# Kernel optimization log

Hardware: AMD Instinct MI355X
Metric: run time of the kernel (lower is better)

The kernel has to match this reference:

```python
import jax, jax.numpy as jnp
import numpy as np
import math

B, L, DIM = 2, 2048, 1024
HEADS = 16
DH = DIM // HEADS  # 64
M_IALSH = 2
U_IALSH = 0.75
NEG = -1e4  # additive mask value for non-matching hash buckets


def setup_inputs() -> dict:
    key = jax.random.key(0)
    k0, k1, k2, k3 = jax.random.split(key, 4)
    return {
        "hidden_states": jax.random.normal(k0, (B, L, DIM), jnp.float32),
        "qk_w": jax.random.normal(k1, (DIM, DIM), jnp.float32) * 0.02,
        "qk_b": jnp.zeros((DIM,), jnp.float32),
        "v_w": jax.random.normal(k2, (DIM, DIM), jnp.float32) * 0.02,
        "v_b": jnp.zeros((DIM,), jnp.float32),
        "hash_a": jax.random.normal(k3, (DH + M_IALSH,), jnp.float32),
    }


def _ialsh_mask(qkh, hash_a):
    # qkh: (b, h, l, dh). IALSH (Improved Asymmetric LSH for MIPS):
    # keys scaled so max norm per (b,h) is U; P(x)=[x, 1/2-||x||^2, 1/2-||x||^4]
    # queries unit-normalized;        Q(x)=[x/||x||, 0, 0]
    norms = jnp.linalg.norm(qkh, axis=-1, keepdims=True)          # (b,h,l,1)
    max_norm = jnp.max(norms, axis=2, keepdims=True)              # (b,h,1,1)
    xk = qkh * (U_IALSH / jnp.maximum(max_norm, 1e-12))
    nk2 = jnp.sum(xk * xk, axis=-1, keepdims=True)                # ||x||^2
    P = jnp.concatenate([xk, 0.5 - nk2, 0.5 - nk2 * nk2], axis=-1)
    q_unit = qkh / jnp.maximum(norms, 1e-12)
    zeros = jnp.zeros_like(nk2)
    Q = jnp.concatenate([q_unit, zeros, zeros], axis=-1)
    hq = (Q @ hash_a) >= 0.0                                      # (b,h,l) sign hash
    hk = (P @ hash_a) >= 0.0
    same = hq[..., :, None] == hk[..., None, :]                   # (b,h,l,l)
    return jnp.where(same, 0.0, NEG).astype(qkh.dtype)


def reference(hidden_states, qk_w, qk_b, v_w, v_b, hash_a):
    b, l, d = hidden_states.shape
    qk = hidden_states @ qk_w.T + qk_b                            # shared Q/K projection
    v = hidden_states @ v_w.T + v_b

    def split(x):  # (b,l,d) -> (b,h,l,dh)
        return x.reshape(b, l, HEADS, DH).transpose(0, 2, 1, 3)

    qkh, vh = split(qk), split(v)
    scores = jnp.einsum('bhqd,bhkd->bhqk', qkh, qkh) / math.sqrt(DH)
    scores = scores + _ialsh_mask(qkh, hash_a)
    probs = jax.nn.softmax(scores, axis=-1)  # dropout = identity (eval mode)
    ctx = jnp.einsum('bhqk,bhkd->bhqd', probs, vh)
    return ctx.transpose(0, 2, 1, 3).reshape(b, l, d)
```

## Files before the change

kernel.cpp:

```cpp
#include <hip/hip_runtime.h>

typedef unsigned short u16;
typedef unsigned char  u8;
typedef unsigned int   u32;

typedef short bf16x8 __attribute__((ext_vector_type(8)));
typedef float f32x4  __attribute__((ext_vector_type(4)));

#define DEV __device__ __forceinline__

#if __has_builtin(__builtin_amdgcn_exp2f)
#define EXP2(x) __builtin_amdgcn_exp2f(x)
#else
#define EXP2(x) exp2f(x)
#endif

DEV u16 f2bf(float x) {
  u32 u = __builtin_bit_cast(u32, x);
  u32 r = (u + 0x7fffu + ((u >> 16) & 1u)) >> 16;
  return (u16)r;
}
DEV float bf2f(u16 h) {
  u32 u = ((u32)h) << 16;
  return __builtin_bit_cast(float, u);
}
DEV f32x4 mfma16(bf16x8 a, bf16x8 b, f32x4 c) {
  return __builtin_amdgcn_mfma_f32_16x16x32_bf16(a, b, c, 0, 0, 0);
}

__global__ __launch_bounds__(256) void split_kernel(
    const float* __restrict__ x, u16* __restrict__ hi, u16* __restrict__ lo, int n) {
  int i = blockIdx.x * 256 + threadIdx.x;
  if (i >= n) return;
  float v = x[i];
  u16 h = f2bf(v);
  hi[i] = h;
  lo[i] = f2bf(v - bf2f(h));
}

__global__ __launch_bounds__(256) void ca_kernel(
    const float* __restrict__ W, const float* __restrict__ ha, double* __restrict__ ca) {
  int idx = blockIdx.x * 256 + threadIdx.x;
  int h = idx >> 10, k = idx & 1023;
  double s = 0.0;
#pragma unroll 8
  for (int j = 0; j < 64; ++j)
    s += (double)W[(size_t)(h * 64 + j) * 1024 + k] * (double)ha[j];
  ca[idx] = s;
}

__global__ __launch_bounds__(256) void d_kernel(
    const float* __restrict__ hid, const double* __restrict__ ca, float* __restrict__ dq) {
  const int row  = blockIdx.x * 4 + (threadIdx.x >> 6);
  const int lane = threadIdx.x & 63;
  const int b = row >> 11, l = row & 2047;
  double acc[16];
#pragma unroll
  for (int h = 0; h < 16; ++h) acc[h] = 0.0;
  const float* hp = hid + (size_t)row * 1024;
  for (int k = lane; k < 1024; k += 64) {
    const double hv = (double)hp[k];
#pragma unroll
    for (int h = 0; h < 16; ++h) acc[h] += hv * ca[h * 1024 + k];
  }
#pragma unroll
  for (int h = 0; h < 16; ++h) {
    double v = acc[h];
#pragma unroll
    for (int off = 32; off; off >>= 1) v += __shfl_xor(v, off, 64);
    if (lane == 0) dq[(size_t)(b * 16 + h) * 2048 + l] = (float)v;
  }
}

__global__ __launch_bounds__(256) void gemm_fused(
    const u16* __restrict__ hHi, const u16* __restrict__ hLo,
    const u16* __restrict__ wqHi, const u16* __restrict__ wqLo,
    const u16* __restrict__ wvHi,
    const float* __restrict__ qk_b, const float* __restrict__ v_b,
    u16* __restrict__ qkB, u16* __restrict__ vB, float* __restrict__ n2A) {
  constexpr int K = 1024, N = 1024;
  __shared__ u16 Ah[128 * 32];
  __shared__ u16 Bh[128 * 32];
  __shared__ u16 Al[128 * 32];
  __shared__ u16 Bl[128 * 32];

  const int zsel = blockIdx.z;
  const u16* __restrict__ Ahi = hHi;
  const u16* __restrict__ Bhi = zsel ? wvHi : wqHi;
  const float* __restrict__ bias = zsel ? v_b : qk_b;
  u16* __restrict__ Cb = zsel ? vB : qkB;
  const int terms = zsel ? 1 : 3;

  const int tid = threadIdx.x;
  const int wave = tid >> 6, lane = tid & 63;
  const int quad = lane >> 4, lm = lane & 15;
  const int wr = wave >> 1, wc = wave & 1;
  const int m0 = blockIdx.x * 128, n0 = blockIdx.y * 128;

  f32x4 acc[4][4];
#pragma unroll
  for (int i = 0; i < 4; ++i)
#pragma unroll
    for (int j = 0; j < 4; ++j) acc[i][j] = {0.f, 0.f, 0.f, 0.f};

  for (int k0 = 0; k0 < K; k0 += 32) {
    __syncthreads();
#pragma unroll
    for (int it = 0; it < 2; ++it) {
      const int rb = wave * 2 + it;
      const int row = rb * 16 + (lane >> 2);
      const int ch = lane & 3;
      const size_t goffA = (size_t)(m0 + row) * K + k0 + ch * 8;
      const size_t goffB = (size_t)(n0 + row) * K + k0 + ch * 8;
      __builtin_amdgcn_global_load_lds(
          (const __attribute__((address_space(1))) void*)(Ahi + goffA),
          (__attribute__((address_space(3))) void*)(Ah + rb * 512), 16, 0, 0);
      __builtin_amdgcn_global_load_lds(
          (const __attribute__((address_space(1))) void*)(Bhi + goffB),
          (__attribute__((address_space(3))) void*)(Bh + rb * 512), 16, 0, 0);
      if (terms > 1) {
        __builtin_amdgcn_global_load_lds(
            (const __attribute__((address_space(1))) void*)(hLo + goffA),
            (__attribute__((address_space(3))) void*)(Al + rb * 512), 16, 0, 0);
        __builtin_amdgcn_global_load_lds(
            (const __attribute__((address_space(1))) void*)(wqLo + goffB),
            (__attribute__((address_space(3))) void*)(Bl + rb * 512), 16, 0, 0);
      }
    }
    __syncthreads();

    bf16x8 a_h[4], b_h[4], a_l[4], b_l[4];
#pragma unroll
    for (int i = 0; i < 4; ++i)
      a_h[i] = *(const bf16x8*)(Ah + (wr * 64 + i * 16 + lm) * 32 + quad * 8);
#pragma unroll
    for (int j = 0; j < 4; ++j)
      b_h[j] = *(const bf16x8*)(Bh + (wc * 64 + j * 16 + lm) * 32 + quad * 8);
    if (terms > 1) {
#pragma unroll
      for (int i = 0; i < 4; ++i)
        a_l[i] = *(const bf16x8*)(Al + (wr * 64 + i * 16 + lm) * 32 + quad * 8);
#pragma unroll
      for (int j = 0; j < 4; ++j)
        b_l[j] = *(const bf16x8*)(Bl + (wc * 64 + j * 16 + lm) * 32 + quad * 8);
    }
    if (terms > 1) {
#pragma unroll
      for (int i = 0; i < 4; ++i)
#pragma unroll
        for (int j = 0; j < 4; ++j) {
          acc[i][j] = mfma16(a_h[i], b_h[j], acc[i][j]);
          acc[i][j] = mfma16(a_h[i], b_l[j], acc[i][j]);
          acc[i][j] = mfma16(a_l[i], b_h[j], acc[i][j]);
        }
    } else {
#pragma unroll
      for (int i = 0; i < 4; ++i)
#pragma unroll
        for (int j = 0; j < 4; ++j)
          acc[i][j] = mfma16(a_h[i], b_h[j], acc[i][j]);
    }
  }

  const int hidx = blockIdx.y * 2 + wc;
#pragma unroll
  for (int i = 0; i < 4; ++i) {
    float nn[4] = {0.f, 0.f, 0.f, 0.f};
#pragma unroll
    for (int j = 0; j < 4; ++j) {
      const int col = n0 + wc * 64 + j * 16 + lm;
      const float bv = bias[col];
#pragma unroll
      for (int r = 0; r < 4; ++r) {
        const int row = m0 + wr * 64 + i * 16 + quad * 4 + r;
        const float val = acc[i][j][r] + bv;
        Cb[(size_t)row * N + col] = f2bf(val);
        nn[r] += val * val;
      }
    }
    if (zsel == 0) {
#pragma unroll
      for (int r = 0; r < 4; ++r)
#pragma unroll
        for (int off = 1; off < 16; off <<= 1) nn[r] += __shfl_xor(nn[r], off, 64);
      if (lm == 0) {
        const int row = m0 + wr * 64 + i * 16 + quad * 4;
        const int b = row >> 11, l = row & 2047;
        *(float4*)&n2A[(size_t)(b * 16 + hidx) * 2048 + l] =
            make_float4(nn[0], nn[1], nn[2], nn[3]);
      }
    }
  }
}

__global__ __launch_bounds__(256) void vtrans_kernel(
    const u16* __restrict__ vB, u16* __restrict__ vT) {
  constexpr int TS = 72;
  __shared__ u16 Ts[64 * TS];
  const int kt = blockIdx.x, bh = blockIdx.y;
  const int b = bh >> 4, h = bh & 15;
  const int tid = threadIdx.x;
  const int row0 = tid >> 3, ch = tid & 7;
  const u16* src = vB + (size_t)b * 2048 * 1024 + h * 64;
#pragma unroll
  for (int it = 0; it < 2; ++it) {
    const int kr = row0 + it * 32;
    uint4 v = *(const uint4*)(src + (size_t)(kt * 64 + kr) * 1024 + ch * 8);
    *(uint4*)((char*)Ts + kr * (TS * 2) + ch * 16) = v;
  }
  __syncthreads();
  u16* dst = vT + (size_t)bh * 64 * 2048 + kt * 64;
#pragma unroll
  for (int it = 0; it < 2; ++it) {
    const int d = row0 + it * 32;
    union { uint4 v; u16 s[8]; } u;
#pragma unroll
    for (int j = 0; j < 8; ++j) u.s[j] = Ts[(ch * 8 + j) * TS + d];
    *(uint4*)(dst + (size_t)d * 2048 + ch * 8) = u.v;
  }
}

__global__ __launch_bounds__(256) void bits_kernel(
    const float* __restrict__ n2A, const float* __restrict__ dq,
    const float* __restrict__ ha, u8* __restrict__ hqA, u8* __restrict__ hkA) {
  const int bh = blockIdx.x;
  const int tid = threadIdx.x;
  const int wave = tid >> 6, lane = tid & 63;
  __shared__ float red[4];
  const float* n2p = n2A + (size_t)bh * 2048;
  float4 v0 = ((const float4*)n2p)[tid];
  float4 v1 = ((const float4*)n2p)[tid + 256];
  float lmax = fmaxf(fmaxf(fmaxf(v0.x, v0.y), fmaxf(v0.z, v0.w)),
                     fmaxf(fmaxf(v1.x, v1.y), fmaxf(v1.z, v1.w)));
#pragma unroll
  for (int off = 1; off < 64; off <<= 1) lmax = fmaxf(lmax, __shfl_xor(lmax, off, 64));
  if (lane == 0) red[wave] = lmax;
  __syncthreads();
  const float maxn2 = fmaxf(fmaxf(red[0], red[1]), fmaxf(red[2], red[3]));
  const float s = 0.75f / fmaxf(sqrtf(maxn2), 1e-12f);
  const float a64 = ha[64], a65 = ha[65];
#pragma unroll
  for (int it = 0; it < 8; ++it) {
    const int l = it * 256 + tid;
    const float dv = dq[(size_t)bh * 2048 + l];
    const float n2 = n2p[l];
    const float nk2 = s * s * n2;
    const float hkdot = s * dv + (0.5f - nk2) * a64 + (0.5f - nk2 * nk2) * a65;
    hqA[(size_t)bh * 2048 + l] = (dv >= 0.f) ? 1 : 0;
    hkA[(size_t)bh * 2048 + l] = (hkdot >= 0.f) ? 1 : 0;
  }
}

__global__ __launch_bounds__(256, 3) void attn_kernel(
    const u16* __restrict__ qkb, const u16* __restrict__ vT,
    const u8* __restrict__ hqA, const u8* __restrict__ hkA, float* __restrict__ out) {
  __shared__ u16 Ks[2][4096];
  __shared__ u16 Vs[2][4096];
  __shared__ u16 Ps[4][2048];

  const int qt = blockIdx.x;
  const int bh = blockIdx.y;
  const int b = bh >> 4, h = bh & 15;
  const int tid = threadIdx.x, wave = tid >> 6, lane = tid & 63;
  const int quad = lane >> 4, lm = lane & 15;
  const int lx = lm & 7;
  const int r8 = lane >> 3, ch = lane & 7;
  const int q0 = qt * 128;

  const u16* qbase = qkb + (size_t)b * 2048 * 1024 + h * 64;
  const u16* vtb = vT + (size_t)bh * 64 * 2048;
  const u8* hkp = hkA + (size_t)bh * 2048;

  bf16x8 aQ[2][2];
#pragma unroll
  for (int s = 0; s < 2; ++s)
#pragma unroll
    for (int c = 0; c < 2; ++c)
      aQ[s][c] = *(const bf16x8*)(qbase +
          (size_t)(q0 + wave * 32 + s * 16 + lm) * 1024 + c * 32 + quad * 8);
  u8 hqb[2][4];
  {
    const u8* hqp = hqA + (size_t)bh * 2048 + q0 + wave * 32;
#pragma unroll
    for (int s = 0; s < 2; ++s)
#pragma unroll
      for (int r = 0; r < 4; ++r) hqb[s][r] = hqp[s * 16 + quad * 4 + r];
  }

  const int srow = wave * 16;
  auto stage = [&](int kt, int buf) {
#pragma unroll
    for (int i = 0; i < 2; ++i) {
      const int row = srow + i * 8 + r8;
      const int sw = (ch ^ (row & 7)) * 8;
      __builtin_amdgcn_global_load_lds(
          (const __attribute__((address_space(1))) void*)(
              qbase + (size_t)(kt * 64 + row) * 1024 + sw),
          (__attribute__((address_space(3))) void*)(&Ks[buf][(srow + i * 8) * 64]),
          16, 0, 0);
      __builtin_amdgcn_global_load_lds(
          (const __attribute__((address_space(1))) void*)(
              vtb + (size_t)row * 2048 + kt * 64 + sw),
          (__attribute__((address_space(3))) void*)(&Vs[buf][(srow + i * 8) * 64]),
          16, 0, 0);
    }
  };

  stage(0, 0);

  f32x4 acc_o[2][4], accL[2];
#pragma unroll
  for (int s = 0; s < 2; ++s) {
    accL[s] = {0.f, 0.f, 0.f, 0.f};
#pragma unroll
    for (int j = 0; j < 4; ++j) acc_o[s][j] = {0.f, 0.f, 0.f, 0.f};
  }
  const bf16x8 ones = {0x3F80, 0x3F80, 0x3F80, 0x3F80, 0x3F80, 0x3F80, 0x3F80, 0x3F80};
  const float SCL = 0.18033688f;
  const float M0 = -4.3280854f;
  const float M1 = -1.4430768e4f;

  __syncthreads();

  for (int kt = 0; kt < 32; ++kt) {
    const int cur = kt & 1;
    if (kt < 31) stage(kt + 1, cur ^ 1);

    u8 hkv[4];
#pragma unroll
    for (int nb = 0; nb < 4; ++nb) hkv[nb] = hkp[kt * 64 + nb * 16 + lm];

    f32x4 cs[2][4];
#pragma unroll
    for (int s = 0; s < 2; ++s)
#pragma unroll
      for (int nb = 0; nb < 4; ++nb) cs[s][nb] = {0.f, 0.f, 0.f, 0.f};
#pragma unroll
    for (int c = 0; c < 2; ++c)
#pragma unroll
      for (int nb = 0; nb < 4; ++nb) {
        bf16x8 bK = *(const bf16x8*)&Ks[cur][(nb * 16 + lm) * 64 + (((c * 4 + quad) ^ lx) * 8)];
        cs[0][nb] = mfma16(aQ[0][c], bK, cs[0][nb]);
        cs[1][nb] = mfma16(aQ[1][c], bK, cs[1][nb]);
      }

#pragma unroll
    for (int s = 0; s < 2; ++s)
#pragma unroll
      for (int nb = 0; nb < 4; ++nb)
#pragma unroll
        for (int r = 0; r < 4; ++r) {
          const float msel = (hqb[s][r] == hkv[nb]) ? M0 : M1;
          const float p = EXP2(__builtin_fmaf(cs[s][nb][r], SCL, msel));
          const int prow = s * 16 + quad * 4 + r;
          const int pc = (nb * 2 + (lm >> 3)) ^ (prow & 7);
          union { float f; u16 hw[2]; } u;
          u.f = p;
          Ps[wave][prow * 64 + pc * 8 + lx] = u.hw[1];
        }

    bf16x8 aP[2][2];
#pragma unroll
    for (int s = 0; s < 2; ++s)
#pragma unroll
      for (int c = 0; c < 2; ++c) {
        aP[s][c] = *(const bf16x8*)&Ps[wave][(s * 16 + lm) * 64 + (((c * 4 + quad) ^ lx) * 8)];
        accL[s] = mfma16(aP[s][c], ones, accL[s]);
      }
#pragma unroll
    for (int c = 0; c < 2; ++c)
#pragma unroll
      for (int j = 0; j < 4; ++j) {
        bf16x8 bV = *(const bf16x8*)&Vs[cur][(j * 16 + lm) * 64 + (((c * 4 + quad) ^ lx) * 8)];
        acc_o[0][j] = mfma16(aP[0][c], bV, acc_o[0][j]);
        acc_o[1][j] = mfma16(aP[1][c], bV, acc_o[1][j]);
      }

    __syncthreads();
  }

#pragma unroll
  for (int s = 0; s < 2; ++s)
#pragma unroll
    for (int r = 0; r < 4; ++r) {
      const float inv = 1.0f / accL[s][r];
      float* op = out + (size_t)(b * 2048 + q0 + wave * 32 + s * 16 + quad * 4 + r) * 1024 + h * 64;
#pragma unroll
      for (int j = 0; j < 4; ++j) op[j * 16 + lm] = acc_o[s][j][r] * inv;
    }
}

extern "C" void kernel_launch(void* const* d_in, const int* in_sizes, int n_in,
                              void* d_out, int out_size, void* d_ws, size_t ws_size,
                              hipStream_t stream) {
  const float* hidden = (const float*)d_in[0];
  const float* qk_w   = (const float*)d_in[1];
  const float* qk_b   = (const float*)d_in[2];
  const float* v_w    = (const float*)d_in[3];
  const float* v_b    = (const float*)d_in[4];
  const float* hash_a = (const float*)d_in[5];
  float* out = (float*)d_out;

  char* base = (char*)d_ws;
  size_t off = 0;
  auto take = [&](size_t bytes) -> char* {
    char* r = base + off;
    off += (bytes + 255) & ~(size_t)255;
    return r;
  };
  const size_t NH = 4194304;
  const size_t NW = 1048576;
  u16* hHi  = (u16*)take(NH * 2);
  u16* hLo  = (u16*)take(NH * 2);
  u16* wqHi = (u16*)take(NW * 2);
  u16* wqLo = (u16*)take(NW * 2);
  u16* wvHi = (u16*)take(NW * 2);
  u16* wvLo = (u16*)take(NW * 2);
  u16* qkB  = (u16*)take(NH * 2);
  u16* vB   = (u16*)take(NH * 2);
  u16* vT   = (u16*)take(NH * 2);
  double* ca = (double*)take(16 * 1024 * 8);
  float* dq  = (float*)take(65536 * 4);
  float* n2A = (float*)take(65536 * 4);
  u8* hqA = (u8*)take(65536);
  u8* hkA = (u8*)take(65536);

  hipLaunchKernelGGL(split_kernel, dim3(NH / 256), dim3(256), 0, stream, hidden, hHi, hLo, (int)NH);
  hipLaunchKernelGGL(split_kernel, dim3(NW / 256), dim3(256), 0, stream, qk_w, wqHi, wqLo, (int)NW);
  hipLaunchKernelGGL(split_kernel, dim3(NW / 256), dim3(256), 0, stream, v_w, wvHi, wvLo, (int)NW);
  hipLaunchKernelGGL(ca_kernel, dim3(64), dim3(256), 0, stream, qk_w, hash_a, ca);
  hipLaunchKernelGGL(d_kernel, dim3(1024), dim3(256), 0, stream, hidden, ca, dq);
  hipLaunchKernelGGL(gemm_fused, dim3(32, 8, 2), dim3(256), 0, stream,
                     hHi, hLo, wqHi, wqLo, wvHi, qk_b, v_b, qkB, vB, n2A);
  hipLaunchKernelGGL(vtrans_kernel, dim3(32, 32), dim3(256), 0, stream, vB, vT);
  hipLaunchKernelGGL(bits_kernel, dim3(32), dim3(256), 0, stream, n2A, dq, hash_a, hqA, hkA);
  hipLaunchKernelGGL(attn_kernel, dim3(16, 32), dim3(256), 0, stream, qkB, vT, hqA, hkA, out);
}
```

Baseline: 257.0 us.

## Compute V transposed directly in GEMM and halve attention query tile

```diff
diff --git a/kernel.cpp b/kernel.cpp
--- a/kernel.cpp
+++ b/kernel.cpp
@@ -77,25 +77,26 @@
     const u16* __restrict__ wqHi, const u16* __restrict__ wqLo,
     const u16* __restrict__ wvHi,
     const float* __restrict__ qk_b, const float* __restrict__ v_b,
-    u16* __restrict__ qkB, u16* __restrict__ vB, float* __restrict__ n2A) {
-  constexpr int K = 1024, N = 1024;
+    u16* __restrict__ qkB, u16* __restrict__ vT, float* __restrict__ n2A) {
+  constexpr int K = 1024;
   __shared__ u16 Ah[128 * 32];
   __shared__ u16 Bh[128 * 32];
   __shared__ u16 Al[128 * 32];
   __shared__ u16 Bl[128 * 32];
 
   const int zsel = blockIdx.z;
-  const u16* __restrict__ Ahi = hHi;
-  const u16* __restrict__ Bhi = zsel ? wvHi : wqHi;
-  const float* __restrict__ bias = zsel ? v_b : qk_b;
-  u16* __restrict__ Cb = zsel ? vB : qkB;
+  const int m0 = (zsel ? blockIdx.y : blockIdx.x) * 128;
+  const int n0 = (zsel ? blockIdx.x : blockIdx.y) * 128;
+  const int CN = zsel ? 4096 : 1024;
+  const u16* __restrict__ Ahi = zsel ? wvHi : hHi;
+  const u16* __restrict__ Bhi = zsel ? hHi : wqHi;
+  u16* __restrict__ Cb = zsel ? vT : qkB;
   const int terms = zsel ? 1 : 3;
 
   const int tid = threadIdx.x;
   const int wave = tid >> 6, lane = tid & 63;
   const int quad = lane >> 4, lm = lane & 15;
   const int wr = wave >> 1, wc = wave & 1;
-  const int m0 = blockIdx.x * 128, n0 = blockIdx.y * 128;
 
   f32x4 acc[4][4];
 #pragma unroll
@@ -143,8 +144,6 @@
 #pragma unroll
       for (int j = 0; j < 4; ++j)
         b_l[j] = *(const bf16x8*)(Bl + (wc * 64 + j * 16 + lm) * 32 + quad * 8);
-    }
-    if (terms > 1) {
 #pragma unroll
       for (int i = 0; i < 4; ++i)
 #pragma unroll
@@ -162,23 +161,23 @@
     }
   }
 
-  const int hidx = blockIdx.y * 2 + wc;
-#pragma unroll
-  for (int i = 0; i < 4; ++i) {
-    float nn[4] = {0.f, 0.f, 0.f, 0.f};
-#pragma unroll
-    for (int j = 0; j < 4; ++j) {
-      const int col = n0 + wc * 64 + j * 16 + lm;
-      const float bv = bias[col];
-#pragma unroll
-      for (int r = 0; r < 4; ++r) {
-        const int row = m0 + wr * 64 + i * 16 + quad * 4 + r;
-        const float val = acc[i][j][r] + bv;
-        Cb[(size_t)row * N + col] = f2bf(val);
-        nn[r] += val * val;
-      }
-    }
-    if (zsel == 0) {
+  if (zsel == 0) {
+    const int hidx = blockIdx.y * 2 + wc;
+#pragma unroll
+    for (int i = 0; i < 4; ++i) {
+      float nn[4] = {0.f, 0.f, 0.f, 0.f};
+#pragma unroll
+      for (int j = 0; j < 4; ++j) {
+        const int col = n0 + wc * 64 + j * 16 + lm;
+        const float bv = qk_b[col];
+#pragma unroll
+        for (int r = 0; r < 4; ++r) {
+          const int row = m0 + wr * 64 + i * 16 + quad * 4 + r;
+          const float val = acc[i][j][r] + bv;
+          Cb[(size_t)row * CN + col] = f2bf(val);
+          nn[r] += val * val;
+        }
+      }
 #pragma unroll
       for (int r = 0; r < 4; ++r)
 #pragma unroll
@@ -190,33 +189,19 @@
             make_float4(nn[0], nn[1], nn[2], nn[3]);
       }
     }
-  }
-}
-
-__global__ __launch_bounds__(256) void vtrans_kernel(
-    const u16* __restrict__ vB, u16* __restrict__ vT) {
-  constexpr int TS = 72;
-  __shared__ u16 Ts[64 * TS];
-  const int kt = blockIdx.x, bh = blockIdx.y;
-  const int b = bh >> 4, h = bh & 15;
-  const int tid = threadIdx.x;
-  const int row0 = tid >> 3, ch = tid & 7;
-  const u16* src = vB + (size_t)b * 2048 * 1024 + h * 64;
-#pragma unroll
-  for (int it = 0; it < 2; ++it) {
-    const int kr = row0 + it * 32;
-    uint4 v = *(const uint4*)(src + (size_t)(kt * 64 + kr) * 1024 + ch * 8);
-    *(uint4*)((char*)Ts + kr * (TS * 2) + ch * 16) = v;
-  }
-  __syncthreads();
-  u16* dst = vT + (size_t)bh * 64 * 2048 + kt * 64;
-#pragma unroll
-  for (int it = 0; it < 2; ++it) {
-    const int d = row0 + it * 32;
-    union { uint4 v; u16 s[8]; } u;
-#pragma unroll
-    for (int j = 0; j < 8; ++j) u.s[j] = Ts[(ch * 8 + j) * TS + d];
-    *(uint4*)(dst + (size_t)d * 2048 + ch * 8) = u.v;
+  } else {
+#pragma unroll
+    for (int i = 0; i < 4; ++i)
+#pragma unroll
+      for (int r = 0; r < 4; ++r) {
+        const int row = m0 + wr * 64 + i * 16 + quad * 4 + r;
+        const float bv = v_b[row];
+#pragma unroll
+        for (int j = 0; j < 4; ++j) {
+          const int col = n0 + wc * 64 + j * 16 + lm;
+          Cb[(size_t)row * CN + col] = f2bf(acc[i][j][r] + bv);
+        }
+      }
   }
 }
 
@@ -251,12 +236,12 @@
   }
 }
 
-__global__ __launch_bounds__(256, 3) void attn_kernel(
+__global__ __launch_bounds__(256, 4) void attn_kernel(
     const u16* __restrict__ qkb, const u16* __restrict__ vT,
     const u8* __restrict__ hqA, const u8* __restrict__ hkA, float* __restrict__ out) {
   __shared__ u16 Ks[2][4096];
   __shared__ u16 Vs[2][4096];
-  __shared__ u16 Ps[4][2048];
+  __shared__ u16 Ps[4][1024];
 
   const int qt = blockIdx.x;
   const int bh = blockIdx.y;
@@ -265,26 +250,22 @@
   const int quad = lane >> 4, lm = lane & 15;
   const int lx = lm & 7;
   const int r8 = lane >> 3, ch = lane & 7;
-  const int q0 = qt * 128;
+  const int q0 = qt * 64;
 
   const u16* qbase = qkb + (size_t)b * 2048 * 1024 + h * 64;
-  const u16* vtb = vT + (size_t)bh * 64 * 2048;
+  const u16* vtb = vT + (size_t)h * 64 * 4096 + b * 2048;
   const u8* hkp = hkA + (size_t)bh * 2048;
 
-  bf16x8 aQ[2][2];
-#pragma unroll
-  for (int s = 0; s < 2; ++s)
-#pragma unroll
-    for (int c = 0; c < 2; ++c)
-      aQ[s][c] = *(const bf16x8*)(qbase +
-          (size_t)(q0 + wave * 32 + s * 16 + lm) * 1024 + c * 32 + quad * 8);
-  u8 hqb[2][4];
+  bf16x8 aQ[2];
+#pragma unroll
+  for (int c = 0; c < 2; ++c)
+    aQ[c] = *(const bf16x8*)(qbase +
+        (size_t)(q0 + wave * 16 + lm) * 1024 + c * 32 + quad * 8);
+  u8 hqb[4];
   {
-    const u8* hqp = hqA + (size_t)bh * 2048 + q0 + wave * 32;
-#pragma unroll
-    for (int s = 0; s < 2; ++s)
-#pragma unroll
-      for (int r = 0; r < 4; ++r) hqb[s][r] = hqp[s * 16 + quad * 4 + r];
+    const u8* hqp = hqA + (size_t)bh * 2048 + q0 + wave * 16;
+#pragma unroll
+    for (int r = 0; r < 4; ++r) hqb[r] = hqp[quad * 4 + r];
   }
 
   const int srow = wave * 16;
@@ -300,7 +281,7 @@
           16, 0, 0);
       __builtin_amdgcn_global_load_lds(
           (const __attribute__((address_space(1))) void*)(
-              vtb + (size_t)row * 2048 + kt * 64 + sw),
+              vtb + (size_t)row * 4096 + kt * 64 + sw),
           (__attribute__((address_space(3))) void*)(&Vs[buf][(srow + i * 8) * 64]),
           16, 0, 0);
     }
@@ -308,13 +289,10 @@
 
   stage(0, 0);
 
-  f32x4 acc_o[2][4], accL[2];
-#pragma unroll
-  for (int s = 0; s < 2; ++s) {
-    accL[s] = {0.f, 0.f, 0.f, 0.f};
-#pragma unroll
-    for (int j = 0; j < 4; ++j) acc_o[s][j] = {0.f, 0.f, 0.f, 0.f};
-  }
+  f32x4 acc_o[4], accL;
+  accL = {0.f, 0.f, 0.f, 0.f};
+#pragma unroll
+  for (int j = 0; j < 4; ++j) acc_o[j] = {0.f, 0.f, 0.f, 0.f};
   const bf16x8 ones = {0x3F80, 0x3F80, 0x3F80, 0x3F80, 0x3F80, 0x3F80, 0x3F80, 0x3F80};
   const float SCL = 0.18033688f;
   const float M0 = -4.3280854f;
@@ -330,64 +308,54 @@
 #pragma unroll
     for (int nb = 0; nb < 4; ++nb) hkv[nb] = hkp[kt * 64 + nb * 16 + lm];
 
-    f32x4 cs[2][4];
-#pragma unroll
-    for (int s = 0; s < 2; ++s)
-#pragma unroll
-      for (int nb = 0; nb < 4; ++nb) cs[s][nb] = {0.f, 0.f, 0.f, 0.f};
+    f32x4 cs[4];
+#pragma unroll
+    for (int nb = 0; nb < 4; ++nb) cs[nb] = {0.f, 0.f, 0.f, 0.f};
 #pragma unroll
     for (int c = 0; c < 2; ++c)
 #pragma unroll
       for (int nb = 0; nb < 4; ++nb) {
         bf16x8 bK = *(const bf16x8*)&Ks[cur][(nb * 16 + lm) * 64 + (((c * 4 + quad) ^ lx) * 8)];
-        cs[0][nb] = mfma16(aQ[0][c], bK, cs[0][nb]);
-        cs[1][nb] = mfma16(aQ[1][c], bK, cs[1][nb]);
-      }
-
-#pragma unroll
-    for (int s = 0; s < 2; ++s)
-#pragma unroll
-      for (int nb = 0; nb < 4; ++nb)
-#pragma unroll
-        for (int r = 0; r < 4; ++r) {
-          const float msel = (hqb[s][r] == hkv[nb]) ? M0 : M1;
-          const float p = EXP2(__builtin_fmaf(cs[s][nb][r], SCL, msel));
-          const int prow = s * 16 + quad * 4 + r;
-          const int pc = (nb * 2 + (lm >> 3)) ^ (prow & 7);
-          union { float f; u16 hw[2]; } u;
-          u.f = p;
-          Ps[wave][prow * 64 + pc * 8 + lx] = u.hw[1];
-        }
-
-    bf16x8 aP[2][2];
-#pragma unroll
-    for (int s = 0; s < 2; ++s)
-#pragma unroll
-      for (int c = 0; c < 2; ++c) {
-        aP[s][c] = *(const bf16x8*)&Ps[wave][(s * 16 + lm) * 64 + (((c * 4 + quad) ^ lx) * 8)];
-        accL[s] = mfma16(aP[s][c], ones, accL[s]);
-      }
+        cs[nb] = mfma16(aQ[c], bK, cs[nb]);
+      }
+
+#pragma unroll
+    for (int nb = 0; nb < 4; ++nb)
+#pragma unroll
+      for (int r = 0; r < 4; ++r) {
+        const float msel = (hqb[r] == hkv[nb]) ? M0 : M1;
+        const float p = EXP2(__builtin_fmaf(cs[nb][r], SCL, msel));
+        const int prow = quad * 4 + r;
+        const int pc = (nb * 2 + (lm >> 3)) ^ (prow & 7);
+        union { float f; u16 hw[2]; } u;
+        u.f = p;
+        Ps[wave][prow * 64 + pc * 8 + lx] = u.hw[1];
+      }
+
+    bf16x8 aP[2];
+#pragma unroll
+    for (int c = 0; c < 2; ++c) {
+      aP[c] = *(const bf16x8*)&Ps[wave][lm * 64 + (((c * 4 + quad) ^ lx) * 8)];
+      accL = mfma16(aP[c], ones, accL);
+    }
 #pragma unroll
     for (int c = 0; c < 2; ++c)
 #pragma unroll
       for (int j = 0; j < 4; ++j) {
         bf16x8 bV = *(const bf16x8*)&Vs[cur][(j * 16 + lm) * 64 + (((c * 4 + quad) ^ lx) * 8)];
-        acc_o[0][j] = mfma16(aP[0][c], bV, acc_o[0][j]);
-        acc_o[1][j] = mfma16(aP[1][c], bV, acc_o[1][j]);
+        acc_o[j] = mfma16(aP[c], bV, acc_o[j]);
       }
 
     __syncthreads();
   }
 
 #pragma unroll
-  for (int s = 0; s < 2; ++s)
-#pragma unroll
-    for (int r = 0; r < 4; ++r) {
-      const float inv = 1.0f / accL[s][r];
-      float* op = out + (size_t)(b * 2048 + q0 + wave * 32 + s * 16 + quad * 4 + r) * 1024 + h * 64;
-#pragma unroll
-      for (int j = 0; j < 4; ++j) op[j * 16 + lm] = acc_o[s][j][r] * inv;
-    }
+  for (int r = 0; r < 4; ++r) {
+    const float inv = 1.0f / accL[r];
+    float* op = out + (size_t)(b * 2048 + q0 + wave * 16 + quad * 4 + r) * 1024 + h * 64;
+#pragma unroll
+    for (int j = 0; j < 4; ++j) op[j * 16 + lm] = acc_o[j][r] * inv;
+  }
 }
 
 extern "C" void kernel_launch(void* const* d_in, const int* in_sizes, int n_in,
@@ -417,7 +385,6 @@
   u16* wvHi = (u16*)take(NW * 2);
   u16* wvLo = (u16*)take(NW * 2);
   u16* qkB  = (u16*)take(NH * 2);
-  u16* vB   = (u16*)take(NH * 2);
   u16* vT   = (u16*)take(NH * 2);
   double* ca = (double*)take(16 * 1024 * 8);
   float* dq  = (float*)take(65536 * 4);
@@ -431,8 +398,7 @@
   hipLaunchKernelGGL(ca_kernel, dim3(64), dim3(256), 0, stream, qk_w, hash_a, ca);
   hipLaunchKernelGGL(d_kernel, dim3(1024), dim3(256), 0, stream, hidden, ca, dq);
   hipLaunchKernelGGL(gemm_fused, dim3(32, 8, 2), dim3(256), 0, stream,
-                     hHi, hLo, wqHi, wqLo, wvHi, qk_b, v_b, qkB, vB, n2A);
-  hipLaunchKernelGGL(vtrans_kernel, dim3(32, 32), dim3(256), 0, stream, vB, vT);
+                     hHi, hLo, wqHi, wqLo, wvHi, qk_b, v_b, qkB, vT, n2A);
   hipLaunchKernelGGL(bits_kernel, dim3(32), dim3(256), 0, stream, n2A, dq, hash_a, hqA, hkA);
-  hipLaunchKernelGGL(attn_kernel, dim3(16, 32), dim3(256), 0, stream, qkB, vT, hqA, hkA, out);
-}
+  hipLaunchKernelGGL(attn_kernel, dim3(32, 32), dim3(256), 0, stream, qkB, vT, hqA, hkA, out);
+}
```

Measured after the change: 245.8 us. 1.05x faster.
